# Kernel optimization log

Hardware: AMD Instinct MI355X
Metric: run time of the kernel (lower is better)

## Reference

```python
import math
import jax, jax.numpy as jnp
import numpy as np

K_MODES = 8
L_ITERS = 8
ALPHA_INIT = 2000.0
TAU_INIT = 0.01


def setup_inputs() -> dict:
    key = jax.random.key(0)
    B, T, C = 64, 4096, 16
    x = jax.random.normal(key, (B, T, C), dtype=jnp.float32)
    log_alpha = jnp.full((L_ITERS, K_MODES), math.log(ALPHA_INIT), dtype=jnp.float32)
    raw_tau = jnp.full((L_ITERS,), math.log(math.expm1(TAU_INIT) + 1e-08), dtype=jnp.float32)
    omega_init = np.linspace(0.05, 0.45, K_MODES)
    raw_omega = jnp.asarray(np.log(2.0 * omega_init / (1.0 - 2.0 * omega_init + 1e-08)), dtype=jnp.float32)
    return {"x": x, "log_alpha": log_alpha, "raw_tau": raw_tau, "raw_omega": raw_omega}


def reference(x, log_alpha, raw_tau, raw_omega):
    B, T, C = x.shape
    L, K = log_alpha.shape
    T_rfft = T // 2 + 1

    alpha = jnp.exp(log_alpha)                    # (L, K)
    tau = jax.nn.softplus(raw_tau)                # (L,)
    omega = jax.nn.sigmoid(raw_omega) * 0.5       # (K,)

    freqs = jnp.linspace(0.0, 0.5, T_rfft, dtype=x.dtype)  # (T_rfft,)
    # (B, T, C) -> (B*C, T)
    x_bc = jnp.transpose(x, (0, 2, 1)).reshape(B * C, T)
    f_hat = jnp.fft.rfft(x_bc, axis=-1)           # (B*C, T_rfft) complex

    # Precompute all denominators: (L, K, T_rfft)
    denom = 1.0 + 2.0 * alpha[:, :, None] * (freqs[None, None, :] - omega[None, :, None]) ** 2

    u0 = jnp.zeros((B * C, K, T_rfft), dtype=f_hat.dtype)
    lam0 = jnp.zeros_like(f_hat)

    def step(carry, per_layer):
        u, lam = carry
        den_l, tau_l = per_layer
        u_sum = u.sum(axis=1)  # (B*C, T_rfft)
        # Jacobi update for all K modes simultaneously
        numerator = f_hat[:, None, :] - (u_sum[:, None, :] - u) + 0.5 * lam[:, None, :]
        u_new = numerator / den_l[None, :, :]
        lam_new = lam + tau_l * (f_hat - u_new.sum(axis=1))
        return (u_new, lam_new), None

    (u_final, _), _ = jax.lax.scan(step, (u0, lam0), (denom, tau))

    modes_flat = jnp.fft.irfft(u_final, n=T, axis=-1)  # (B*C, K, T)
    modes = jnp.transpose(modes_flat.reshape(B, C, K, T), (0, 2, 3, 1))  # (B, K, T, C)
    return modes
```

## Files before the change

### kernel.cpp

```cpp
#include <hip/hip_runtime.h>
#include <math.h>

#ifndef M_PI
#define M_PI 3.14159265358979323846
#endif

#define T_LEN 4096
#define M_LEN 2048
#define NFREQ 2049
#define KM 8
#define LI 8
#define CD 16

template <int NT>
__device__ __forceinline__ float2* fft2048(float2* a, float2* b, int tid, float sign) {
    float2* src = a;
    float2* dst = b;
    int l = 1024;
    #pragma unroll 1
    for (int s = 0; s < 11; ++s) {
        float piol = sign * (float)M_PI / (float)l;
        #pragma unroll
        for (int ii = 0; ii < 1024 / NT; ++ii) {
            int i = tid + ii * NT;
            int j = i >> s;
            float2 A = src[i];
            float2 B = src[i + 1024];
            float ang = piol * (float)j;
            float sw, cw;
            __sincosf(ang, &sw, &cw);
            float2 sum = make_float2(A.x + B.x, A.y + B.y);
            float2 dif = make_float2(A.x - B.x, A.y - B.y);
            float2 tw = make_float2(dif.x * cw - dif.y * sw, dif.x * sw + dif.y * cw);
            int p = i + (j << s);
            dst[p] = sum;
            dst[p + (1 << s)] = tw;
        }
        __syncthreads();
        float2* t = src; src = dst; dst = t;
        l >>= 1;
    }
    return src;
}

__global__ void __launch_bounds__(512)
k_fwd_iter(const float* __restrict__ x,
           const float* __restrict__ log_alpha,
           const float* __restrict__ raw_tau,
           const float* __restrict__ raw_omega,
           float2* __restrict__ u_ws)
{
    __shared__ float2 bufA[M_LEN];
    __shared__ float2 bufB[M_LEN];
    __shared__ float s_2a[LI * KM];
    __shared__ float s_tau[LI];
    __shared__ float s_om[KM];

    const int tid = threadIdx.x;
    const int row = blockIdx.x;
    const int b = row >> 4;
    const int c = row & 15;

    if (tid < LI * KM) s_2a[tid] = 2.0f * __expf(log_alpha[tid]);
    if (tid < LI)      s_tau[tid] = log1pf(__expf(raw_tau[tid]));
    if (tid < KM)      s_om[tid]  = 0.5f / (1.0f + __expf(-raw_omega[tid]));

    const float* xr = x + (size_t)b * T_LEN * CD + c;
    #pragma unroll
    for (int q = 0; q < 4; ++q) {
        int n = tid + q * 512;
        float e = xr[(size_t)(2 * n) * CD];
        float o = xr[(size_t)(2 * n + 1) * CD];
        bufA[n] = make_float2(e, o);
    }
    __syncthreads();

    float2* Z = fft2048<512>(bufA, bufB, tid, -1.0f);

    const size_t sb = (size_t)(b * (KM * CD) + c);

    for (int f = tid; f < NFREQ; f += 512) {
        float2 Zk = Z[f & (M_LEN - 1)];
        float2 Zm = Z[(M_LEN - f) & (M_LEN - 1)];
        float2 E = make_float2(0.5f * (Zk.x + Zm.x), 0.5f * (Zk.y - Zm.y));
        float2 D = make_float2(0.5f * (Zk.x - Zm.x), 0.5f * (Zk.y + Zm.y));
        float2 O = make_float2(D.y, -D.x);
        float ang = -2.0f * (float)M_PI * (float)f / (float)T_LEN;
        float sw, cw;
        __sincosf(ang, &sw, &cw);
        float fhx = E.x + cw * O.x - sw * O.y;
        float fhy = E.y + cw * O.y + sw * O.x;

        float freq = (float)f * (0.5f / (float)M_LEN);
        float dd[KM];
        #pragma unroll
        for (int k = 0; k < KM; ++k) {
            float d = freq - s_om[k];
            dd[k] = d * d;
        }

        float2 u[KM];
        #pragma unroll
        for (int k = 0; k < KM; ++k) u[k] = make_float2(0.f, 0.f);
        float lamx = 0.f, lamy = 0.f;

        #pragma unroll
        for (int l = 0; l < LI; ++l) {
            float usx = 0.f, usy = 0.f;
            #pragma unroll
            for (int k = 0; k < KM; ++k) { usx += u[k].x; usy += u[k].y; }
            float bx = fhx - usx + 0.5f * lamx;
            float by = fhy - usy + 0.5f * lamy;
            float sx = 0.f, sy = 0.f;
            #pragma unroll
            for (int k = 0; k < KM; ++k) {
                float den = fmaf(s_2a[l * KM + k], dd[k], 1.0f);
                float r = __builtin_amdgcn_rcpf(den);
                float ux = (bx + u[k].x) * r;
                float uy = (by + u[k].y) * r;
                u[k].x = ux; u[k].y = uy;
                sx += ux; sy += uy;
            }
            lamx += s_tau[l] * (fhx - sx);
            lamy += s_tau[l] * (fhy - sy);
        }

        #pragma unroll
        for (int k = 0; k < KM; ++k) {
            u_ws[(sb + (size_t)k * CD) * NFREQ + f] = u[k];
        }
    }
}

__global__ void __launch_bounds__(1024)
k_inv(const float2* __restrict__ u_ws, float* __restrict__ out)
{
    __shared__ float2 bufA[NFREQ];
    __shared__ float2 bufB[M_LEN];
    const int tid = threadIdx.x;
    const int bk = blockIdx.x;

    float val[CD][4];

    #pragma unroll
    for (int c = 0; c < CD; ++c) {
        const float2* sp = u_ws + (size_t)(bk * CD + c) * NFREQ;
        bufA[tid] = sp[tid];
        bufA[tid + 1024] = sp[tid + 1024];
        if (tid == 0) bufA[2048] = sp[2048];
        __syncthreads();

        #pragma unroll
        for (int jj = 0; jj < 2; ++jj) {
            int j = tid + jj * 1024;
            float2 Xj = bufA[j];
            float2 Xm = bufA[M_LEN - j];
            float2 E = make_float2(0.5f * (Xj.x + Xm.x), 0.5f * (Xj.y - Xm.y));
            float2 D = make_float2(0.5f * (Xj.x - Xm.x), 0.5f * (Xj.y + Xm.y));
            float ang = 2.0f * (float)M_PI * (float)j / (float)T_LEN;
            float sw, cw;
            __sincosf(ang, &sw, &cw);
            float2 O = make_float2(cw * D.x - sw * D.y, cw * D.y + sw * D.x);
            const float sc = 1.0f / (float)M_LEN;
            bufB[j] = make_float2((E.x - O.y) * sc, (E.y + O.x) * sc);
        }
        __syncthreads();

        float2* res = fft2048<1024>(bufB, bufA, tid, 1.0f);
        float2 z0 = res[2 * tid];
        float2 z1 = res[2 * tid + 1];
        val[c][0] = z0.x;
        val[c][1] = z0.y;
        val[c][2] = z1.x;
        val[c][3] = z1.y;
        __syncthreads();
    }

    float4* op = (float4*)(out + ((size_t)bk * T_LEN + (size_t)(4 * tid)) * CD);
    #pragma unroll
    for (int r = 0; r < 4; ++r) {
        #pragma unroll
        for (int g = 0; g < 4; ++g) {
            op[r * 4 + g] = make_float4(val[4 * g + 0][r], val[4 * g + 1][r],
                                        val[4 * g + 2][r], val[4 * g + 3][r]);
        }
    }
}

extern "C" void kernel_launch(void* const* d_in, const int* in_sizes, int n_in,
                              void* d_out, int out_size, void* d_ws, size_t ws_size,
                              hipStream_t stream) {
    const float* x         = (const float*)d_in[0];
    const float* log_alpha = (const float*)d_in[1];
    const float* raw_tau   = (const float*)d_in[2];
    const float* raw_omega = (const float*)d_in[3];
    float* out = (float*)d_out;
    float2* u_ws = (float2*)d_ws;

    k_fwd_iter<<<dim3(64 * CD), dim3(512), 0, stream>>>(x, log_alpha, raw_tau,
                                                        raw_omega, u_ws);
    k_inv<<<dim3(64 * KM), dim3(1024), 0, stream>>>(u_ws, out);
}
```

Measured before the change: 396.8 us.

## Precompute inverse FFT twiddles, swizzle LDS indices, simplify ADMM first iteration

The inverse kernel now computes its per-stage twiddle factors once per thread before the channel loop instead of calling sincos in every butterfly. The 11 radix-2 stages are fully unrolled with specialized final stages, and an XOR swizzle on shared-memory indices is meant to reduce bank conflicts. The forward ADMM loop peels the first iteration, where u and lambda are zero, and carries the running mode sum and half-lambda directly so the per-step sums and scaling go away. Keeping the precomputed twiddles adds register pressure in the 1024-thread inverse kernel, which already holds a 64-element value array.

```diff
diff --git a/kernel.cpp b/kernel.cpp
--- a/kernel.cpp
+++ b/kernel.cpp
@@ -11,6 +11,8 @@
 #define KM 8
 #define LI 8
 #define CD 16
+
+#define SWZ(i) ((i) ^ (((i) >> 4) & 15))
 
 template <int NT>
 __device__ __forceinline__ float2* fft2048(float2* a, float2* b, int tid, float sign) {
@@ -53,7 +55,7 @@
     __shared__ float2 bufA[M_LEN];
     __shared__ float2 bufB[M_LEN];
     __shared__ float s_2a[LI * KM];
-    __shared__ float s_tau[LI];
+    __shared__ float s_tau2[LI];
     __shared__ float s_om[KM];
 
     const int tid = threadIdx.x;
@@ -61,9 +63,9 @@
     const int b = row >> 4;
     const int c = row & 15;
 
-    if (tid < LI * KM) s_2a[tid] = 2.0f * __expf(log_alpha[tid]);
-    if (tid < LI)      s_tau[tid] = log1pf(__expf(raw_tau[tid]));
-    if (tid < KM)      s_om[tid]  = 0.5f / (1.0f + __expf(-raw_omega[tid]));
+    if (tid < LI * KM) s_2a[tid]   = 2.0f * __expf(log_alpha[tid]);
+    if (tid < LI)      s_tau2[tid] = 0.5f * log1pf(__expf(raw_tau[tid]));
+    if (tid < KM)      s_om[tid]   = 0.5f / (1.0f + __expf(-raw_omega[tid]));
 
     const float* xr = x + (size_t)b * T_LEN * CD + c;
     #pragma unroll
@@ -100,18 +102,30 @@
         }
 
         float2 u[KM];
-        #pragma unroll
-        for (int k = 0; k < KM; ++k) u[k] = make_float2(0.f, 0.f);
-        float lamx = 0.f, lamy = 0.f;
-
-        #pragma unroll
-        for (int l = 0; l < LI; ++l) {
-            float usx = 0.f, usy = 0.f;
+        float sx, sy;
+        float hx, hy;
+
+        {
+            float nsx = 0.f, nsy = 0.f;
             #pragma unroll
-            for (int k = 0; k < KM; ++k) { usx += u[k].x; usy += u[k].y; }
-            float bx = fhx - usx + 0.5f * lamx;
-            float by = fhy - usy + 0.5f * lamy;
-            float sx = 0.f, sy = 0.f;
+            for (int k = 0; k < KM; ++k) {
+                float den = fmaf(s_2a[k], dd[k], 1.0f);
+                float r = __builtin_amdgcn_rcpf(den);
+                float ux = fhx * r;
+                float uy = fhy * r;
+                u[k].x = ux; u[k].y = uy;
+                nsx += ux; nsy += uy;
+            }
+            hx = s_tau2[0] * (fhx - nsx);
+            hy = s_tau2[0] * (fhy - nsy);
+            sx = nsx; sy = nsy;
+        }
+
+        #pragma unroll
+        for (int l = 1; l < LI; ++l) {
+            float bx = fhx - sx + hx;
+            float by = fhy - sy + hy;
+            float nsx = 0.f, nsy = 0.f;
             #pragma unroll
             for (int k = 0; k < KM; ++k) {
                 float den = fmaf(s_2a[l * KM + k], dd[k], 1.0f);
@@ -119,10 +133,11 @@
                 float ux = (bx + u[k].x) * r;
                 float uy = (by + u[k].y) * r;
                 u[k].x = ux; u[k].y = uy;
-                sx += ux; sy += uy;
+                nsx += ux; nsy += uy;
             }
-            lamx += s_tau[l] * (fhx - sx);
-            lamy += s_tau[l] * (fhy - sy);
+            hx += s_tau2[l] * (fhx - nsx);
+            hy += s_tau2[l] * (fhy - nsy);
+            sx = nsx; sy = nsy;
         }
 
         #pragma unroll
@@ -130,6 +145,40 @@
             u_ws[(sb + (size_t)k * CD) * NFREQ + f] = u[k];
         }
     }
+}
+
+#define R2STAGE(S, SRC, DST, CW, SN) {                                        \
+    int j_ = tid >> (S);                                                      \
+    float2 A_ = SRC[SWZ(tid)];                                                \
+    float2 B_ = SRC[SWZ(tid + 1024)];                                         \
+    float2 sum_ = make_float2(A_.x + B_.x, A_.y + B_.y);                      \
+    float2 dif_ = make_float2(A_.x - B_.x, A_.y - B_.y);                      \
+    float2 tw_ = make_float2(dif_.x * (CW) - dif_.y * (SN),                   \
+                             dif_.x * (SN) + dif_.y * (CW));                  \
+    int p_ = tid + (j_ << (S));                                               \
+    DST[SWZ(p_)] = sum_;                                                      \
+    DST[SWZ(p_ + (1 << (S)))] = tw_;                                          \
+    __syncthreads();                                                          \
+}
+
+#define R2STAGE9(SRC, DST) {                                                  \
+    float2 A_ = SRC[SWZ(tid)];                                                \
+    float2 B_ = SRC[SWZ(tid + 1024)];                                         \
+    float2 sum_ = make_float2(A_.x + B_.x, A_.y + B_.y);                      \
+    float2 dif_ = make_float2(A_.x - B_.x, A_.y - B_.y);                      \
+    float2 tw_ = (tid & 512) ? make_float2(-dif_.y, dif_.x) : dif_;           \
+    int p_ = tid + ((tid >> 9) << 9);                                         \
+    DST[SWZ(p_)] = sum_;                                                      \
+    DST[SWZ(p_ + 512)] = tw_;                                                 \
+    __syncthreads();                                                          \
+}
+
+#define R2STAGE10(SRC, DST) {                                                 \
+    float2 A_ = SRC[SWZ(tid)];                                                \
+    float2 B_ = SRC[SWZ(tid + 1024)];                                         \
+    DST[SWZ(tid)] = make_float2(A_.x + B_.x, A_.y + B_.y);                    \
+    DST[SWZ(tid + 1024)] = make_float2(A_.x - B_.x, A_.y - B_.y);             \
+    __syncthreads();                                                          \
 }
 
 __global__ void __launch_bounds__(1024)
@@ -140,35 +189,61 @@
     const int tid = threadIdx.x;
     const int bk = blockIdx.x;
 
+    float cs0,sn0,cs1,sn1,cs2,sn2,cs3,sn3,cs4,sn4,cs5,sn5,cs6,sn6,cs7,sn7,cs8,sn8;
+    {
+        const float w = (float)M_PI / 1024.0f;
+        __sincosf(w * (float)tid,          &sn0, &cs0);
+        __sincosf(w * (float)(tid & ~1),   &sn1, &cs1);
+        __sincosf(w * (float)(tid & ~3),   &sn2, &cs2);
+        __sincosf(w * (float)(tid & ~7),   &sn3, &cs3);
+        __sincosf(w * (float)(tid & ~15),  &sn4, &cs4);
+        __sincosf(w * (float)(tid & ~31),  &sn5, &cs5);
+        __sincosf(w * (float)(tid & ~63),  &sn6, &cs6);
+        __sincosf(w * (float)(tid & ~127), &sn7, &cs7);
+        __sincosf(w * (float)(tid & ~255), &sn8, &cs8);
+    }
+    float csR, snR;
+    __sincosf(((float)M_PI / 2048.0f) * (float)tid, &snR, &csR);
+
     float val[CD][4];
 
     #pragma unroll
     for (int c = 0; c < CD; ++c) {
         const float2* sp = u_ws + (size_t)(bk * CD + c) * NFREQ;
-        bufA[tid] = sp[tid];
-        bufA[tid + 1024] = sp[tid + 1024];
+        bufA[SWZ(tid)] = sp[tid];
+        bufA[SWZ(tid + 1024)] = sp[tid + 1024];
         if (tid == 0) bufA[2048] = sp[2048];
         __syncthreads();
 
+        const float sc = 1.0f / (float)M_LEN;
         #pragma unroll
         for (int jj = 0; jj < 2; ++jj) {
             int j = tid + jj * 1024;
-            float2 Xj = bufA[j];
-            float2 Xm = bufA[M_LEN - j];
+            float cw = jj ? -snR : csR;
+            float sw = jj ?  csR : snR;
+            float2 Xj = bufA[SWZ(j)];
+            float2 Xm = (j > 0) ? bufA[SWZ(M_LEN - j)] : bufA[2048];
             float2 E = make_float2(0.5f * (Xj.x + Xm.x), 0.5f * (Xj.y - Xm.y));
             float2 D = make_float2(0.5f * (Xj.x - Xm.x), 0.5f * (Xj.y + Xm.y));
-            float ang = 2.0f * (float)M_PI * (float)j / (float)T_LEN;
-            float sw, cw;
-            __sincosf(ang, &sw, &cw);
             float2 O = make_float2(cw * D.x - sw * D.y, cw * D.y + sw * D.x);
-            const float sc = 1.0f / (float)M_LEN;
-            bufB[j] = make_float2((E.x - O.y) * sc, (E.y + O.x) * sc);
-        }
-        __syncthreads();
-
-        float2* res = fft2048<1024>(bufB, bufA, tid, 1.0f);
-        float2 z0 = res[2 * tid];
-        float2 z1 = res[2 * tid + 1];
+            bufB[SWZ(j)] = make_float2((E.x - O.y) * sc, (E.y + O.x) * sc);
+        }
+        __syncthreads();
+
+        R2STAGE(0, bufB, bufA, cs0, sn0);
+        R2STAGE(1, bufA, bufB, cs1, sn1);
+        R2STAGE(2, bufB, bufA, cs2, sn2);
+        R2STAGE(3, bufA, bufB, cs3, sn3);
+        R2STAGE(4, bufB, bufA, cs4, sn4);
+        R2STAGE(5, bufA, bufB, cs5, sn5);
+        R2STAGE(6, bufB, bufA, cs6, sn6);
+        R2STAGE(7, bufA, bufB, cs7, sn7);
+        R2STAGE(8, bufB, bufA, cs8, sn8);
+        R2STAGE9(bufA, bufB);
+        R2STAGE10(bufB, bufA);
+
+        float2 z0 = bufA[SWZ(2 * tid)];
+        float2 z1 = bufA[SWZ(2 * tid + 1)];
         val[c][0] = z0.x;
         val[c][1] = z0.y;
         val[c][2] = z1.x;
```

Measured after the change: 352.3 us. 1.13x faster.
